# Kernel optimization log

Hardware: AMD Instinct MI355X
Metric: run time of the kernel (lower is better)

Reference implementation:

```python
import jax, jax.numpy as jnp
import numpy as np

DIM = 256
HEADS = 8
H = 32
W = 32
N = H * W  # must equal 4*DIM for the BatchNorm1d(dim*4) over the token dim to be valid
TAU = 2.0
V_TH = 1.0


def _rope_rotations():
    # RoPE buffer: shape (H, W, DIM//2) angles; k_max = DIM // (2*2)
    k_max = DIM // 4
    theta = 1.0 / (10000.0 ** (jnp.arange(k_max, dtype=jnp.float32) / k_max))
    hg, wg = jnp.meshgrid(jnp.arange(H, dtype=jnp.float32), jnp.arange(W, dtype=jnp.float32), indexing='ij')
    angles = jnp.concatenate([hg[..., None] * theta, wg[..., None] * theta], axis=-1)  # (H,W,DIM//2)
    return jnp.cos(angles), jnp.sin(angles)


def _apply_rope(x, cos, sin):
    # x: (b,H,W,DIM); complex rotation on consecutive (re,im) pairs
    x2 = x.reshape(*x.shape[:-1], -1, 2)
    re, im = x2[..., 0], x2[..., 1]
    out = jnp.stack([cos * re - sin * im, sin * re + cos * im], axis=-1)
    return out.reshape(x.shape)


def _lif(x):
    # MultiStepLIFNode(tau=2.0, detach_reset=True): time axis = axis 0 (here batch, as in source),
    # decay_input=True, v_reset=0 (hard reset), heaviside fwd + sigmoid(alpha=4) surrogate bwd.
    def step(v, xt):
        v = v + (xt - v) / TAU
        sg = jax.nn.sigmoid(4.0 * (v - V_TH))
        spike = jax.lax.stop_gradient((v >= V_TH).astype(x.dtype) - sg) + sg
        v = v * (1.0 - jax.lax.stop_gradient(spike))  # detach_reset hard reset to 0
        return v, spike
    _, s = jax.lax.scan(step, jnp.zeros_like(x[0]), x)
    return s


def setup_inputs() -> dict:
    key = jax.random.key(0)
    ks = jax.random.split(key, 4)
    x = jax.random.normal(ks[0], (8, N, DIM), dtype=jnp.float32)
    Wqk = jax.random.normal(ks[1], (DIM, 2 * DIM), dtype=jnp.float32) * 0.02
    bqk = jnp.zeros((2 * DIM,), dtype=jnp.float32)
    bn_gamma = jnp.ones((N,), dtype=jnp.float32)
    bn_beta = jnp.zeros((N,), dtype=jnp.float32)
    lepe_w = jax.random.normal(ks[2], (DIM, 1, 3, 3), dtype=jnp.float32) * 0.1
    lepe_b = jnp.zeros((DIM,), dtype=jnp.float32)
    return {"x": x, "Wqk": Wqk, "bqk": bqk, "bn_gamma": bn_gamma, "bn_beta": bn_beta,
            "lepe_w": lepe_w, "lepe_b": lepe_b}


def reference(x, Wqk, bqk, bn_gamma, bn_beta, lepe_w, lepe_b):
    b, n, c = x.shape
    hd = c // HEADS
    cos, sin = _rope_rotations()

    qk = x @ Wqk + bqk  # (b,n,2c)
    # Dropout is identity in eval. BatchNorm1d(4*dim) in eval mode: channels = token dim (n == 4*dim),
    # running_mean=0, running_var=1 -> pure affine per token index.
    qk = qk * bn_gamma[None, :, None] + bn_beta[None, :, None]
    qk = _lif(qk)
    q, k = qk[..., :c], qk[..., c:]  # reshape(b,n,2,c) split
    v = x
    q = jax.nn.elu(q) + 1.0
    k = jax.nn.elu(k) + 1.0

    q_rope = _apply_rope(q.reshape(b, H, W, c), cos, sin).reshape(b, n, HEADS, hd).transpose(0, 2, 1, 3)
    k_rope = _apply_rope(k.reshape(b, H, W, c), cos, sin).reshape(b, n, HEADS, hd).transpose(0, 2, 1, 3)
    qh = q.reshape(b, n, HEADS, hd).transpose(0, 2, 1, 3)  # (b,h,n,d)
    kh = k.reshape(b, n, HEADS, hd).transpose(0, 2, 1, 3)
    vh = v.reshape(b, n, HEADS, hd).transpose(0, 2, 1, 3)

    atten = jnp.einsum('bhnd,bhmd->bhnm', qh, kh)  # returned, not used for output
    kmean = kh.mean(axis=2, keepdims=True)  # (b,h,1,d)
    z = 1.0 / (jnp.einsum('bhnd,bhed->bhne', qh, kmean) + 1e-6)  # (b,h,n,1)
    kv = jnp.einsum('bhnd,bhne->bhde', k_rope, vh) / n  # (k^T n^-0.5) @ (v n^-0.5)
    out = jnp.einsum('bhnd,bhde->bhne', q_rope, kv) * z  # (b,h,n,d)
    out = out.transpose(0, 2, 1, 3).reshape(b, n, c)

    v_img = vh.transpose(0, 2, 1, 3).reshape(b, H, W, c).transpose(0, 3, 1, 2)  # (b,c,H,W)
    lepe = jax.lax.conv_general_dilated(v_img, lepe_w, (1, 1), 'SAME',
                                        feature_group_count=c,
                                        dimension_numbers=('NCHW', 'OIHW', 'NCHW'))
    lepe = lepe + lepe_b[None, :, None, None]
    out = out + lepe.transpose(0, 2, 3, 1).reshape(b, n, c)
    return (out, qh, kh, v_img, atten)
```

## Files before the change

### kernel.cpp

```cpp
#include <hip/hip_runtime.h>
#include <cstdint>
#include <cstddef>

#define OFF_OUT   0
#define OFF_QH    2097152
#define OFF_KH    4194304
#define OFF_VIMG  6291456
#define OFF_ATT   8388608

#define WS_MQ   0
#define WS_MK   65536
#define WS_TBL  131072
#define WS_KVP  393216
#define WS_KMP  655360

typedef float f32x4 __attribute__((ext_vector_type(4)));

__global__ __launch_bounds__(512) void phase1_kernel(
    const float* __restrict__ x, const float* __restrict__ Wqk,
    const float* __restrict__ bqk, const float* __restrict__ gamma,
    const float* __restrict__ beta, unsigned* __restrict__ mq,
    unsigned* __restrict__ mk, float* __restrict__ vimg,
    float* __restrict__ tbl)
{
    __shared__ float smem[12800];
    __shared__ unsigned nib[8][4][8][8];
    int t = threadIdx.x;
    int blk = blockIdx.x;

    if (blk >= 1536) {
        int id = (blk - 1536) * 512 + t;
        int j = id & 127, n = id >> 7;
        int i = (j < 64) ? j : j - 64;
        float th = powf(10000.0f, -(float)i * (1.0f / 64.0f));
        float pos = (float)((j < 64) ? (n >> 5) : (n & 31));
        float ang = pos * th;
        tbl[n * 256 + j * 2]     = cosf(ang);
        tbl[n * 256 + j * 2 + 1] = sinf(ang);
        return;
    }
    if (blk >= 512) {
        int tile = (blk - 512) * 2 + (t >> 8);
        int st = t & 255;
        float* s = smem + (t >> 8) * 1056;
        int b = tile >> 8, ti = tile & 255;
        int p0 = (ti >> 3) * 32, c0 = (ti & 7) * 32;
        int row = st >> 3, c4 = (st & 7) * 4;
        const float4 vl = *(const float4*)&x[(b * 1024 + p0 + row) * 256 + c0 + c4];
        s[row * 33 + c4 + 0] = vl.x; s[row * 33 + c4 + 1] = vl.y;
        s[row * 33 + c4 + 2] = vl.z; s[row * 33 + c4 + 3] = vl.w;
        __syncthreads();
        int cc = st >> 3, p4 = (st & 7) * 4;
        f32x4 o;
        o.x = s[(p4 + 0) * 33 + cc]; o.y = s[(p4 + 1) * 33 + cc];
        o.z = s[(p4 + 2) * 33 + cc]; o.w = s[(p4 + 3) * 33 + cc];
        __builtin_nontemporal_store(o, (f32x4*)&vimg[(b * 256 + c0 + cc) * 1024 + p0 + p4]);
        return;
    }

    int ks = t >> 8, tl = t & 255;
    int blk_n = blk >> 2, blk_c = blk & 3;
    int n0 = blk_n * 8, c0 = blk_c * 128;
    int c_t = tl & 31, n_l = tl >> 5;
    float* xs  = smem + ks * 2176;
    float* wsb = smem + 4352 + ks * 4224;

    float acc[8][4];
    #pragma unroll
    for (int b = 0; b < 8; ++b)
        #pragma unroll
        for (int j = 0; j < 4; ++j) acc[b][j] = 0.f;

    int um = tl >> 3, ukq = tl & 7;
    const float* gx1 = x + ((size_t)(um & 7) * 1024 + n0 + (um >> 3)) * 256 + ks * 128 + ukq * 4;
    const float* gx2 = gx1 + 4 * 256;
    float* lx1 = xs + (ukq * 4) * 68 + um;
    float* lx2 = lx1 + 32;
    const float* gw = Wqk + ((size_t)ks * 128 + (tl >> 5)) * 512 + c0 + (tl & 31) * 4;
    float* lw0 = wsb + (tl >> 5) * 132 + (tl & 31) * 4;

    f32x4 px0, px1, pw0, pw1, pw2, pw3;
    px0 = *(const f32x4*)(gx1);
    px1 = *(const f32x4*)(gx2);
    pw0 = *(const f32x4*)(gw);
    pw1 = *(const f32x4*)(gw + 8 * 512);
    pw2 = *(const f32x4*)(gw + 16 * 512);
    pw3 = *(const f32x4*)(gw + 24 * 512);

    for (int p = 0; p < 4; ++p) {
        #pragma unroll
        for (int j = 0; j < 4; ++j) { lx1[j * 68] = px0[j]; lx2[j * 68] = px1[j]; }
        *(f32x4*)(lw0)            = pw0;
        *(f32x4*)(lw0 + 8 * 132)  = pw1;
        *(f32x4*)(lw0 + 16 * 132) = pw2;
        *(f32x4*)(lw0 + 24 * 132) = pw3;
        __syncthreads();
        if (p < 3) {
            int ko = (p + 1) * 32;
            px0 = *(const f32x4*)(gx1 + ko);
            px1 = *(const f32x4*)(gx2 + ko);
            pw0 = *(const f32x4*)(gw + (ko + 0) * 512);
            pw1 = *(const f32x4*)(gw + (ko + 8) * 512);
            pw2 = *(const f32x4*)(gw + (ko + 16) * 512);
            pw3 = *(const f32x4*)(gw + (ko + 24) * 512);
        }
        #pragma unroll 8
        for (int kk = 0; kk < 32; ++kk) {
            f32x4 xa  = *(const f32x4*)(xs + kk * 68 + n_l * 8);
            f32x4 xb2 = *(const f32x4*)(xs + kk * 68 + n_l * 8 + 4);
            f32x4 w4  = *(const f32x4*)(wsb + kk * 132 + c_t * 4);
            #pragma unroll
            for (int b = 0; b < 4; ++b)
                #pragma unroll
                for (int j = 0; j < 4; ++j)
                    acc[b][j] = fmaf(xa[b], w4[j], acc[b][j]);
            #pragma unroll
            for (int b = 0; b < 4; ++b)
                #pragma unroll
                for (int j = 0; j < 4; ++j)
                    acc[b + 4][j] = fmaf(xb2[b], w4[j], acc[b + 4][j]);
        }
        __syncthreads();
    }

    float* comb = smem;
    if (ks == 1) {
        #pragma unroll
        for (int idx = 0; idx < 32; ++idx)
            comb[idx * 257 + tl] = acc[idx >> 2][idx & 3];
    }
    __syncthreads();
    if (ks == 0) {
        #pragma unroll
        for (int idx = 0; idx < 32; ++idx)
            acc[idx >> 2][idx & 3] += comb[idx * 257 + tl];
        float g = gamma[n0 + n_l], be = beta[n0 + n_l];
        f32x4 bq = *(const f32x4*)&bqk[c0 + c_t * 4];
        float v0 = 0.f, v1 = 0.f, v2 = 0.f, v3 = 0.f;
        #pragma unroll
        for (int b = 0; b < 8; ++b) {
            float a0 = (acc[b][0] + bq[0]) * g + be;
            float a1 = (acc[b][1] + bq[1]) * g + be;
            float a2 = (acc[b][2] + bq[2]) * g + be;
            float a3 = (acc[b][3] + bq[3]) * g + be;
            v0 = v0 + (a0 - v0) * 0.5f; v1 = v1 + (a1 - v1) * 0.5f;
            v2 = v2 + (a2 - v2) * 0.5f; v3 = v3 + (a3 - v3) * 0.5f;
            unsigned s0 = (v0 >= 1.f), s1 = (v1 >= 1.f), s2 = (v2 >= 1.f), s3 = (v3 >= 1.f);
            v0 = s0 ? 0.f : v0; v1 = s1 ? 0.f : v1;
            v2 = s2 ? 0.f : v2; v3 = s3 ? 0.f : v3;
            nib[n_l][c_t >> 3][c_t & 7][b] = s0 | (s1 << 1) | (s2 << 2) | (s3 << 3);
        }
    }
    __syncthreads();
    if (t < 256) {
        int b = t & 7, hp = (t >> 3) & 3, nl = t >> 5;
        unsigned wd = 0;
        #pragma unroll
        for (int c8 = 0; c8 < 8; ++c8)
            wd |= nib[nl][hp][c8][b] << (4 * c8);
        unsigned h = (unsigned)((blk_c & 1) * 4 + hp);
        unsigned* dst = (blk_c < 2) ? mq : mk;
        dst[b * 8192 + h * 1024 + n0 + nl] = wd;
    }
}

__global__ __launch_bounds__(256) void phase2_kernel(
    const unsigned* __restrict__ mq, const unsigned* __restrict__ mk,
    const float* __restrict__ x, const float* __restrict__ tbl,
    float* __restrict__ qh, float* __restrict__ kh, float* __restrict__ att,
    float* __restrict__ kvp, float* __restrict__ kmp)
{
    int t = threadIdx.x;
    if (blockIdx.x < 256) {
        int bh = blockIdx.x >> 2, seg = blockIdx.x & 3;
        int b = bh >> 3, h = bh & 7;
        int n0 = seg * 256;
        __shared__ float part[8][32];
        __shared__ float kr[64][36];
        __shared__ float vhs[64][33];
        int d = t & 31, ch = t >> 5;
        int sc = 0;
        for (int i = 0; i < 32; ++i)
            sc += (mk[bh * 1024 + n0 + ch * 32 + i] >> d) & 1u;
        part[ch][d] = (float)sc;
        __syncthreads();
        if (t < 32) {
            float cs = 0.f;
            #pragma unroll
            for (int j = 0; j < 8; ++j) cs += part[j][t];
            kmp[bh * 128 + seg * 32 + t] = cs;
        }
        float a0 = 0, a1 = 0, a2 = 0, a3 = 0;
        int e = t & 31, db = (t >> 5) * 4;
        for (int c0 = n0; c0 < n0 + 256; c0 += 64) {
            __syncthreads();
            #pragma unroll
            for (int i = 0; i < 8; ++i) {
                int f = t + i * 256;
                int nn = f >> 5, dd = f & 31;
                int n = c0 + nn;
                unsigned w = mk[bh * 1024 + n];
                float kd = 1.0f + (float)((w >> dd) & 1u);
                float ko = 1.0f + (float)((w >> (dd ^ 1)) & 1u);
                const float* cp = tbl + n * 256 + h * 32 + (dd & ~1);
                float cc2 = cp[0], ss2 = cp[1];
                kr[nn][dd] = (dd & 1) ? (ss2 * ko + cc2 * kd) : (cc2 * kd - ss2 * ko);
                vhs[nn][dd] = x[(b * 1024 + n) * 256 + h * 32 + dd];
            }
            __syncthreads();
            #pragma unroll 8
            for (int nn = 0; nn < 64; ++nn) {
                float ve = vhs[nn][e];
                float4 kk = *(const float4*)&kr[nn][db];
                a0 = fmaf(kk.x, ve, a0); a1 = fmaf(kk.y, ve, a1);
                a2 = fmaf(kk.z, ve, a2); a3 = fmaf(kk.w, ve, a3);
            }
        }
        float* dst = kvp + bh * 4096 + seg * 1024;
        dst[(db + 0) * 32 + e] = a0;
        dst[(db + 1) * 32 + e] = a1;
        dst[(db + 2) * 32 + e] = a2;
        dst[(db + 3) * 32 + e] = a3;
        return;
    }
    int blk = blockIdx.x - 256;
    int bh = blk >> 5;
    int tile = blk & 31;
    {
        int row = tile * 32 + (t >> 3);
        int d0 = (t & 7) * 4;
        unsigned wq = mq[bh * 1024 + row], wk = mk[bh * 1024 + row];
        f32x4 a, bb;
        a.x = 1.f + (float)((wq >> (d0 + 0)) & 1u);
        a.y = 1.f + (float)((wq >> (d0 + 1)) & 1u);
        a.z = 1.f + (float)((wq >> (d0 + 2)) & 1u);
        a.w = 1.f + (float)((wq >> (d0 + 3)) & 1u);
        bb.x = 1.f + (float)((wk >> (d0 + 0)) & 1u);
        bb.y = 1.f + (float)((wk >> (d0 + 1)) & 1u);
        bb.z = 1.f + (float)((wk >> (d0 + 2)) & 1u);
        bb.w = 1.f + (float)((wk >> (d0 + 3)) & 1u);
        __builtin_nontemporal_store(a,  (f32x4*)&qh[((bh * 1024 + row) << 5) + d0]);
        __builtin_nontemporal_store(bb, (f32x4*)&kh[((bh * 1024 + row) << 5) + d0]);
    }
    uint4 mm = ((const uint4*)(mk + bh * 1024))[t];
    float4 rr;
    rr.x = (float)__popc(mm.x); rr.y = (float)__popc(mm.y);
    rr.z = (float)__popc(mm.z); rr.w = (float)__popc(mm.w);
    float* base = att + ((size_t)bh * 1024 + (size_t)tile * 32) * 1024;
    for (int row = 0; row < 32; ++row) {
        unsigned mqw = mq[bh * 1024 + tile * 32 + row];
        float rq = 32.0f + (float)__popc(mqw);
        f32x4 o;
        o.x = rq + rr.x + (float)__popc(mqw & mm.x);
        o.y = rq + rr.y + (float)__popc(mqw & mm.y);
        o.z = rq + rr.z + (float)__popc(mqw & mm.z);
        o.w = rq + rr.w + (float)__popc(mqw & mm.w);
        __builtin_nontemporal_store(o, (f32x4*)(base + (size_t)row * 1024) + t);
    }
}

__global__ __launch_bounds__(256) void out_kernel(
    const unsigned* __restrict__ mq, const float* __restrict__ x,
    const float* __restrict__ tbl, const float* __restrict__ kvp,
    const float* __restrict__ kmp, const float* __restrict__ lw,
    const float* __restrict__ lb, float* __restrict__ out)
{
    int t = threadIdx.x;
    int bi = blockIdx.x;
    int bh = bi >> 3, sub = bi & 7;
    int pseg = sub >> 1, half = sub & 1;
    int b = bh >> 3, h = bh & 7;
    bool hy = (h < 4);
    int e = t & 31, p_l = t >> 5;
    int p = pseg * 8 + p_l;
    int q0 = half * 16;

    __shared__ float kvs[32][32];
    __shared__ float kmf[32];
    __shared__ float zs[128];
    const float inv = 1.0f / 1024.0f;
    #pragma unroll
    for (int i = 0; i < 4; ++i) {
        int f = t + i * 256;
        const float* kp = kvp + bh * 4096 + f;
        kvs[f >> 5][f & 31] = (kp[0] + kp[1024] + kp[2048] + kp[3072]) * inv;
    }
    if (t < 32) {
        const float* mp = kmp + bh * 128 + t;
        kmf[t] = 1.0f + (mp[0] + mp[32] + mp[64] + mp[96]) * inv;
    }
    __syncthreads();
    float S = 0.f;
    #pragma unroll
    for (int dd = 0; dd < 32; ++dd) S += kmf[dd];
    if (t < 128) {
        int pl2 = t >> 4, iq = t & 15;
        int pp = pseg * 8 + pl2, qq = q0 + iq;
        int n = hy ? (pp * 32 + qq) : (qq * 32 + pp);
        unsigned w = mq[bh * 1024 + n];
        float acc = S;
        #pragma unroll
        for (int dd = 0; dd < 32; ++dd)
            acc += (float)((w >> dd) & 1u) * kmf[dd];
        zs[t] = 1.0f / (acc + 1e-6f);
    }
    int n_ref = hy ? (p * 32) : p;
    const float* cp = tbl + n_ref * 256 + h * 32;
    float E[16], O[16], B = 0.f;
    #pragma unroll
    for (int j = 0; j < 16; ++j) {
        float c2 = cp[2 * j], s2 = cp[2 * j + 1];
        float K0 = kvs[2 * j][e], K1 = kvs[2 * j + 1][e];
        E[j] = c2 * K0 + s2 * K1;
        O[j] = c2 * K1 - s2 * K0;
        B += E[j] + O[j];
    }
    __syncthreads();
    int c = h * 32 + e;
    float w9[9];
    #pragma unroll
    for (int j = 0; j < 9; ++j) w9[j] = lw[c * 9 + j];
    float lbv = lb[c];
    const float* xb = x + (size_t)b * 262144 + c;
    auto ld = [&](int yy, int xx) -> float {
        if ((unsigned)yy > 31u || (unsigned)xx > 31u) return 0.f;
        return xb[(yy * 32 + xx) * 256];
    };
    if (hy) {
        int y = p;
        float Wm0 = ld(y - 1, q0 - 1), Wm1 = ld(y, q0 - 1), Wm2 = ld(y + 1, q0 - 1);
        float Wc0 = ld(y - 1, q0),     Wc1 = ld(y, q0),     Wc2 = ld(y + 1, q0);
        #pragma unroll 4
        for (int i = 0; i < 16; ++i) {
            int m = q0 + i;
            float Wp0 = ld(y - 1, m + 1), Wp1 = ld(y, m + 1), Wp2 = ld(y + 1, m + 1);
            int n = y * 32 + m;
            unsigned w = mq[bh * 1024 + n];
            float o = B;
            #pragma unroll
            for (int j = 0; j < 16; ++j) {
                o += (float)((w >> (2 * j)) & 1u) * E[j];
                o += (float)((w >> (2 * j + 1)) & 1u) * O[j];
            }
            o *= zs[p_l * 16 + i];
            float l = lbv;
            l = fmaf(w9[0], Wm0, l); l = fmaf(w9[1], Wc0, l); l = fmaf(w9[2], Wp0, l);
            l = fmaf(w9[3], Wm1, l); l = fmaf(w9[4], Wc1, l); l = fmaf(w9[5], Wp1, l);
            l = fmaf(w9[6], Wm2, l); l = fmaf(w9[7], Wc2, l); l = fmaf(w9[8], Wp2, l);
            __builtin_nontemporal_store(o + l, &out[((b * 1024 + n) << 8) + c]);
            Wm0 = Wc0; Wm1 = Wc1; Wm2 = Wc2;
            Wc0 = Wp0; Wc1 = Wp1; Wc2 = Wp2;
        }
    } else {
        int xx0 = p;
        float Wm0 = ld(q0 - 1, xx0 - 1), Wm1 = ld(q0 - 1, xx0), Wm2 = ld(q0 - 1, xx0 + 1);
        float Wc0 = ld(q0, xx0 - 1),     Wc1 = ld(q0, xx0),     Wc2 = ld(q0, xx0 + 1);
        #pragma unroll 4
        for (int i = 0; i < 16; ++i) {
            int m = q0 + i;
            float Wp0 = ld(m + 1, xx0 - 1), Wp1 = ld(m + 1, xx0), Wp2 = ld(m + 1, xx0 + 1);
            int n = m * 32 + xx0;
            unsigned w = mq[bh * 1024 + n];
            float o = B;
            #pragma unroll
            for (int j = 0; j < 16; ++j) {
                o += (float)((w >> (2 * j)) & 1u) * E[j];
                o += (float)((w >> (2 * j + 1)) & 1u) * O[j];
            }
            o *= zs[p_l * 16 + i];
            float l = lbv;
            l = fmaf(w9[0], Wm0, l); l = fmaf(w9[1], Wm1, l); l = fmaf(w9[2], Wm2, l);
            l = fmaf(w9[3], Wc0, l); l = fmaf(w9[4], Wc1, l); l = fmaf(w9[5], Wc2, l);
            l = fmaf(w9[6], Wp0, l); l = fmaf(w9[7], Wp1, l); l = fmaf(w9[8], Wp2, l);
            __builtin_nontemporal_store(o + l, &out[((b * 1024 + n) << 8) + c]);
            Wm0 = Wc0; Wm1 = Wc1; Wm2 = Wc2;
            Wc0 = Wp0; Wc1 = Wp1; Wc2 = Wp2;
        }
    }
}

extern "C" void kernel_launch(void* const* d_in, const int* in_sizes, int n_in,
                              void* d_out, int out_size, void* d_ws, size_t ws_size,
                              hipStream_t stream)
{
    const float* x     = (const float*)d_in[0];
    const float* Wqk   = (const float*)d_in[1];
    const float* bqk   = (const float*)d_in[2];
    const float* gamma = (const float*)d_in[3];
    const float* beta  = (const float*)d_in[4];
    const float* lw    = (const float*)d_in[5];
    const float* lb    = (const float*)d_in[6];
    float* out = (float*)d_out;
    unsigned* ws = (unsigned*)d_ws;
    unsigned* mq = ws + WS_MQ;
    unsigned* mk = ws + WS_MK;
    float* tbl  = (float*)(ws + WS_TBL);
    float* kvp  = (float*)(ws + WS_KVP);
    float* kmp  = (float*)(ws + WS_KMP);

    hipLaunchKernelGGL(phase1_kernel, dim3(1792), dim3(512), 0, stream,
                       x, Wqk, bqk, gamma, beta, mq, mk, out + OFF_VIMG, tbl);
    hipLaunchKernelGGL(phase2_kernel, dim3(2304), dim3(256), 0, stream,
                       mq, mk, x, tbl, out + OFF_QH, out + OFF_KH, out + OFF_ATT,
                       kvp, kmp);
    hipLaunchKernelGGL(out_kernel, dim3(512), dim3(256), 0, stream,
                       mq, x, tbl, kvp, kmp, lw, lb, out + OFF_OUT);
}
```

Before: 107.6 us.

## Reschedule kernels so K-mask GEMM runs first and Q GEMM overlaps KV reduction

The original first kernel computed both the Q and K spike masks, the RoPE table and the v_img transpose. Now phase A computes only the K half of the GEMM/LIF alongside the table and the transpose. Phase B computes the Q half concurrently with the KV/k-mean partial reductions, which need only the K mask. The attention-matrix/qh/kh writes are then fused into the same launch as the final output kernel. The aim is to fill idle CUs by pairing independent work in each launch, at the cost of heavier mixed blocks and a different load balance.

```diff
diff --git a/kernel.cpp b/kernel.cpp
--- a/kernel.cpp
+++ b/kernel.cpp
@@ -16,50 +16,14 @@
 
 typedef float f32x4 __attribute__((ext_vector_type(4)));
 
-__global__ __launch_bounds__(512) void phase1_kernel(
+__device__ __forceinline__ void gemm_lif_512(
     const float* __restrict__ x, const float* __restrict__ Wqk,
     const float* __restrict__ bqk, const float* __restrict__ gamma,
     const float* __restrict__ beta, unsigned* __restrict__ mq,
-    unsigned* __restrict__ mk, float* __restrict__ vimg,
-    float* __restrict__ tbl)
+    unsigned* __restrict__ mk, float* smem, unsigned* nib,
+    int blk_n, int blk_c, int t)
 {
-    __shared__ float smem[12800];
-    __shared__ unsigned nib[8][4][8][8];
-    int t = threadIdx.x;
-    int blk = blockIdx.x;
-
-    if (blk >= 1536) {
-        int id = (blk - 1536) * 512 + t;
-        int j = id & 127, n = id >> 7;
-        int i = (j < 64) ? j : j - 64;
-        float th = powf(10000.0f, -(float)i * (1.0f / 64.0f));
-        float pos = (float)((j < 64) ? (n >> 5) : (n & 31));
-        float ang = pos * th;
-        tbl[n * 256 + j * 2]     = cosf(ang);
-        tbl[n * 256 + j * 2 + 1] = sinf(ang);
-        return;
-    }
-    if (blk >= 512) {
-        int tile = (blk - 512) * 2 + (t >> 8);
-        int st = t & 255;
-        float* s = smem + (t >> 8) * 1056;
-        int b = tile >> 8, ti = tile & 255;
-        int p0 = (ti >> 3) * 32, c0 = (ti & 7) * 32;
-        int row = st >> 3, c4 = (st & 7) * 4;
-        const float4 vl = *(const float4*)&x[(b * 1024 + p0 + row) * 256 + c0 + c4];
-        s[row * 33 + c4 + 0] = vl.x; s[row * 33 + c4 + 1] = vl.y;
-        s[row * 33 + c4 + 2] = vl.z; s[row * 33 + c4 + 3] = vl.w;
-        __syncthreads();
-        int cc = st >> 3, p4 = (st & 7) * 4;
-        f32x4 o;
-        o.x = s[(p4 + 0) * 33 + cc]; o.y = s[(p4 + 1) * 33 + cc];
-        o.z = s[(p4 + 2) * 33 + cc]; o.w = s[(p4 + 3) * 33 + cc];
-        __builtin_nontemporal_store(o, (f32x4*)&vimg[(b * 256 + c0 + cc) * 1024 + p0 + p4]);
-        return;
-    }
-
     int ks = t >> 8, tl = t & 255;
-    int blk_n = blk >> 2, blk_c = blk & 3;
     int n0 = blk_n * 8, c0 = blk_c * 128;
     int c_t = tl & 31, n_l = tl >> 5;
     float* xs  = smem + ks * 2176;
@@ -148,7 +112,8 @@
             unsigned s0 = (v0 >= 1.f), s1 = (v1 >= 1.f), s2 = (v2 >= 1.f), s3 = (v3 >= 1.f);
             v0 = s0 ? 0.f : v0; v1 = s1 ? 0.f : v1;
             v2 = s2 ? 0.f : v2; v3 = s3 ? 0.f : v3;
-            nib[n_l][c_t >> 3][c_t & 7][b] = s0 | (s1 << 1) | (s2 << 2) | (s3 << 3);
+            nib[n_l * 256 + (c_t >> 3) * 64 + (c_t & 7) * 8 + b] =
+                s0 | (s1 << 1) | (s2 << 2) | (s3 << 3);
         }
     }
     __syncthreads();
@@ -157,115 +122,174 @@
         unsigned wd = 0;
         #pragma unroll
         for (int c8 = 0; c8 < 8; ++c8)
-            wd |= nib[nl][hp][c8][b] << (4 * c8);
+            wd |= nib[nl * 256 + hp * 64 + c8 * 8 + b] << (4 * c8);
         unsigned h = (unsigned)((blk_c & 1) * 4 + hp);
         unsigned* dst = (blk_c < 2) ? mq : mk;
         dst[b * 8192 + h * 1024 + n0 + nl] = wd;
     }
 }
 
-__global__ __launch_bounds__(256) void phase2_kernel(
+__global__ __launch_bounds__(512) void phaseA_kernel(
+    const float* __restrict__ x, const float* __restrict__ Wqk,
+    const float* __restrict__ bqk, const float* __restrict__ gamma,
+    const float* __restrict__ beta, unsigned* __restrict__ mq,
+    unsigned* __restrict__ mk, float* __restrict__ vimg,
+    float* __restrict__ tbl)
+{
+    __shared__ float smem[12800];
+    __shared__ unsigned nib[2048];
+    int t = threadIdx.x;
+    int blk = blockIdx.x;
+    if (blk < 256) {
+        gemm_lif_512(x, Wqk, bqk, gamma, beta, mq, mk, smem, nib,
+                     blk >> 1, 2 + (blk & 1), t);
+        return;
+    }
+    if (blk >= 1280) {
+        int id = (blk - 1280) * 512 + t;
+        int j = id & 127, n = id >> 7;
+        int i = (j < 64) ? j : j - 64;
+        float th = powf(10000.0f, -(float)i * (1.0f / 64.0f));
+        float pos = (float)((j < 64) ? (n >> 5) : (n & 31));
+        float ang = pos * th;
+        tbl[n * 256 + j * 2]     = cosf(ang);
+        tbl[n * 256 + j * 2 + 1] = sinf(ang);
+        return;
+    }
+    int tile = (blk - 256) * 2 + (t >> 8);
+    int st = t & 255;
+    float* s = smem + (t >> 8) * 1056;
+    int b = tile >> 8, ti = tile & 255;
+    int p0 = (ti >> 3) * 32, c0 = (ti & 7) * 32;
+    int row = st >> 3, c4 = (st & 7) * 4;
+    const float4 vl = *(const float4*)&x[(b * 1024 + p0 + row) * 256 + c0 + c4];
+    s[row * 33 + c4 + 0] = vl.x; s[row * 33 + c4 + 1] = vl.y;
+    s[row * 33 + c4 + 2] = vl.z; s[row * 33 + c4 + 3] = vl.w;
+    __syncthreads();
+    int cc = st >> 3, p4 = (st & 7) * 4;
+    f32x4 o;
+    o.x = s[(p4 + 0) * 33 + cc]; o.y = s[(p4 + 1) * 33 + cc];
+    o.z = s[(p4 + 2) * 33 + cc]; o.w = s[(p4 + 3) * 33 + cc];
+    __builtin_nontemporal_store(o, (f32x4*)&vimg[(b * 256 + c0 + cc) * 1024 + p0 + p4]);
+}
+
+__global__ __launch_bounds__(512) void phaseB_kernel(
+    const float* __restrict__ x, const float* __restrict__ Wqk,
+    const float* __restrict__ bqk, const float* __restrict__ gamma,
+    const float* __restrict__ beta, unsigned* __restrict__ mq,
+    unsigned* __restrict__ mk, const float* __restrict__ tbl,
+    float* __restrict__ kvp, float* __restrict__ kmp)
+{
+    __shared__ float smem[12800];
+    __shared__ unsigned nib[2048];
+    int t = threadIdx.x;
+    int blk = blockIdx.x;
+    if (blk < 256) {
+        gemm_lif_512(x, Wqk, bqk, gamma, beta, mq, mk, smem, nib,
+                     blk >> 1, blk & 1, t);
+        return;
+    }
+    int ks2 = t >> 8, tl = t & 255;
+    int unit = (blk - 256) * 2 + ks2;
+    int bh = unit >> 2, seg = unit & 3;
+    int b = bh >> 3, h = bh & 7;
+    int n0 = seg * 256;
+    float* kr   = smem + ks2 * 4800;
+    float* vhs  = kr + 2304;
+    float* part = kr + 4416;
+    int d = tl & 31, ch = tl >> 5;
+    int sc = 0;
+    for (int i = 0; i < 32; ++i)
+        sc += (mk[bh * 1024 + n0 + ch * 32 + i] >> d) & 1u;
+    part[ch * 32 + d] = (float)sc;
+    __syncthreads();
+    if (tl < 32) {
+        float cs = 0.f;
+        #pragma unroll
+        for (int j = 0; j < 8; ++j) cs += part[j * 32 + tl];
+        kmp[bh * 128 + seg * 32 + tl] = cs;
+    }
+    float a0 = 0, a1 = 0, a2 = 0, a3 = 0;
+    int e = tl & 31, db = (tl >> 5) * 4;
+    for (int c0 = n0; c0 < n0 + 256; c0 += 64) {
+        __syncthreads();
+        #pragma unroll
+        for (int i = 0; i < 8; ++i) {
+            int f = tl + i * 256;
+            int nn = f >> 5, dd = f & 31;
+            int n = c0 + nn;
+            unsigned w = mk[bh * 1024 + n];
+            float kd = 1.0f + (float)((w >> dd) & 1u);
+            float ko = 1.0f + (float)((w >> (dd ^ 1)) & 1u);
+            const float* cp = tbl + n * 256 + h * 32 + (dd & ~1);
+            float cc2 = cp[0], ss2 = cp[1];
+            kr[nn * 36 + dd] = (dd & 1) ? (ss2 * ko + cc2 * kd) : (cc2 * kd - ss2 * ko);
+            vhs[nn * 33 + dd] = x[(b * 1024 + n) * 256 + h * 32 + dd];
+        }
+        __syncthreads();
+        #pragma unroll 8
+        for (int nn = 0; nn < 64; ++nn) {
+            float ve = vhs[nn * 33 + e];
+            float4 kk = *(const float4*)&kr[nn * 36 + db];
+            a0 = fmaf(kk.x, ve, a0); a1 = fmaf(kk.y, ve, a1);
+            a2 = fmaf(kk.z, ve, a2); a3 = fmaf(kk.w, ve, a3);
+        }
+    }
+    float* dst = kvp + bh * 4096 + seg * 1024;
+    dst[(db + 0) * 32 + e] = a0;
+    dst[(db + 1) * 32 + e] = a1;
+    dst[(db + 2) * 32 + e] = a2;
+    dst[(db + 3) * 32 + e] = a3;
+}
+
+__global__ __launch_bounds__(256) void phaseC_kernel(
     const unsigned* __restrict__ mq, const unsigned* __restrict__ mk,
     const float* __restrict__ x, const float* __restrict__ tbl,
-    float* __restrict__ qh, float* __restrict__ kh, float* __restrict__ att,
-    float* __restrict__ kvp, float* __restrict__ kmp)
+    const float* __restrict__ kvp, const float* __restrict__ kmp,
+    const float* __restrict__ lw, const float* __restrict__ lb,
+    float* __restrict__ outbase)
 {
     int t = threadIdx.x;
-    if (blockIdx.x < 256) {
-        int bh = blockIdx.x >> 2, seg = blockIdx.x & 3;
-        int b = bh >> 3, h = bh & 7;
-        int n0 = seg * 256;
-        __shared__ float part[8][32];
-        __shared__ float kr[64][36];
-        __shared__ float vhs[64][33];
-        int d = t & 31, ch = t >> 5;
-        int sc = 0;
-        for (int i = 0; i < 32; ++i)
-            sc += (mk[bh * 1024 + n0 + ch * 32 + i] >> d) & 1u;
-        part[ch][d] = (float)sc;
-        __syncthreads();
-        if (t < 32) {
-            float cs = 0.f;
-            #pragma unroll
-            for (int j = 0; j < 8; ++j) cs += part[j][t];
-            kmp[bh * 128 + seg * 32 + t] = cs;
-        }
-        float a0 = 0, a1 = 0, a2 = 0, a3 = 0;
-        int e = t & 31, db = (t >> 5) * 4;
-        for (int c0 = n0; c0 < n0 + 256; c0 += 64) {
-            __syncthreads();
-            #pragma unroll
-            for (int i = 0; i < 8; ++i) {
-                int f = t + i * 256;
-                int nn = f >> 5, dd = f & 31;
-                int n = c0 + nn;
-                unsigned w = mk[bh * 1024 + n];
-                float kd = 1.0f + (float)((w >> dd) & 1u);
-                float ko = 1.0f + (float)((w >> (dd ^ 1)) & 1u);
-                const float* cp = tbl + n * 256 + h * 32 + (dd & ~1);
-                float cc2 = cp[0], ss2 = cp[1];
-                kr[nn][dd] = (dd & 1) ? (ss2 * ko + cc2 * kd) : (cc2 * kd - ss2 * ko);
-                vhs[nn][dd] = x[(b * 1024 + n) * 256 + h * 32 + dd];
-            }
-            __syncthreads();
-            #pragma unroll 8
-            for (int nn = 0; nn < 64; ++nn) {
-                float ve = vhs[nn][e];
-                float4 kk = *(const float4*)&kr[nn][db];
-                a0 = fmaf(kk.x, ve, a0); a1 = fmaf(kk.y, ve, a1);
-                a2 = fmaf(kk.z, ve, a2); a3 = fmaf(kk.w, ve, a3);
-            }
-        }
-        float* dst = kvp + bh * 4096 + seg * 1024;
-        dst[(db + 0) * 32 + e] = a0;
-        dst[(db + 1) * 32 + e] = a1;
-        dst[(db + 2) * 32 + e] = a2;
-        dst[(db + 3) * 32 + e] = a3;
+    if (blockIdx.x >= 512) {
+        int blk = blockIdx.x - 512;
+        int bh = blk >> 5;
+        int tile = blk & 31;
+        float* qh = outbase + OFF_QH;
+        float* kh = outbase + OFF_KH;
+        float* att = outbase + OFF_ATT;
+        {
+            int row = tile * 32 + (t >> 3);
+            int d0 = (t & 7) * 4;
+            unsigned wq = mq[bh * 1024 + row], wk = mk[bh * 1024 + row];
+            f32x4 a, bb;
+            a.x = 1.f + (float)((wq >> (d0 + 0)) & 1u);
+            a.y = 1.f + (float)((wq >> (d0 + 1)) & 1u);
+            a.z = 1.f + (float)((wq >> (d0 + 2)) & 1u);
+            a.w = 1.f + (float)((wq >> (d0 + 3)) & 1u);
+            bb.x = 1.f + (float)((wk >> (d0 + 0)) & 1u);
+            bb.y = 1.f + (float)((wk >> (d0 + 1)) & 1u);
+            bb.z = 1.f + (float)((wk >> (d0 + 2)) & 1u);
+            bb.w = 1.f + (float)((wk >> (d0 + 3)) & 1u);
+            __builtin_nontemporal_store(a,  (f32x4*)&qh[((bh * 1024 + row) << 5) + d0]);
+            __builtin_nontemporal_store(bb, (f32x4*)&kh[((bh * 1024 + row) << 5) + d0]);
+        }
+        uint4 mm = ((const uint4*)(mk + bh * 1024))[t];
+        float4 rr;
+        rr.x = (float)__popc(mm.x); rr.y = (float)__popc(mm.y);
+        rr.z = (float)__popc(mm.z); rr.w = (float)__popc(mm.w);
+        float* base = att + ((size_t)bh * 1024 + (size_t)tile * 32) * 1024;
+        for (int row = 0; row < 32; ++row) {
+            unsigned mqw = mq[bh * 1024 + tile * 32 + row];
+            float rq = 32.0f + (float)__popc(mqw);
+            f32x4 o;
+            o.x = rq + rr.x + (float)__popc(mqw & mm.x);
+            o.y = rq + rr.y + (float)__popc(mqw & mm.y);
+            o.z = rq + rr.z + (float)__popc(mqw & mm.z);
+            o.w = rq + rr.w + (float)__popc(mqw & mm.w);
+            __builtin_nontemporal_store(o, (f32x4*)(base + (size_t)row * 1024) + t);
+        }
         return;
     }
-    int blk = blockIdx.x - 256;
-    int bh = blk >> 5;
-    int tile = blk & 31;
-    {
-        int row = tile * 32 + (t >> 3);
-        int d0 = (t & 7) * 4;
-        unsigned wq = mq[bh * 1024 + row], wk = mk[bh * 1024 + row];
-        f32x4 a, bb;
-        a.x = 1.f + (float)((wq >> (d0 + 0)) & 1u);
-        a.y = 1.f + (float)((wq >> (d0 + 1)) & 1u);
-        a.z = 1.f + (float)((wq >> (d0 + 2)) & 1u);
-        a.w = 1.f + (float)((wq >> (d0 + 3)) & 1u);
-        bb.x = 1.f + (float)((wk >> (d0 + 0)) & 1u);
-        bb.y = 1.f + (float)((wk >> (d0 + 1)) & 1u);
-        bb.z = 1.f + (float)((wk >> (d0 + 2)) & 1u);
-        bb.w = 1.f + (float)((wk >> (d0 + 3)) & 1u);
-        __builtin_nontemporal_store(a,  (f32x4*)&qh[((bh * 1024 + row) << 5) + d0]);
-        __builtin_nontemporal_store(bb, (f32x4*)&kh[((bh * 1024 + row) << 5) + d0]);
-    }
-    uint4 mm = ((const uint4*)(mk + bh * 1024))[t];
-    float4 rr;
-    rr.x = (float)__popc(mm.x); rr.y = (float)__popc(mm.y);
-    rr.z = (float)__popc(mm.z); rr.w = (float)__popc(mm.w);
-    float* base = att + ((size_t)bh * 1024 + (size_t)tile * 32) * 1024;
-    for (int row = 0; row < 32; ++row) {
-        unsigned mqw = mq[bh * 1024 + tile * 32 + row];
-        float rq = 32.0f + (float)__popc(mqw);
-        f32x4 o;
-        o.x = rq + rr.x + (float)__popc(mqw & mm.x);
-        o.y = rq + rr.y + (float)__popc(mqw & mm.y);
-        o.z = rq + rr.z + (float)__popc(mqw & mm.z);
-        o.w = rq + rr.w + (float)__popc(mqw & mm.w);
-        __builtin_nontemporal_store(o, (f32x4*)(base + (size_t)row * 1024) + t);
-    }
-}
-
-__global__ __launch_bounds__(256) void out_kernel(
-    const unsigned* __restrict__ mq, const float* __restrict__ x,
-    const float* __restrict__ tbl, const float* __restrict__ kvp,
-    const float* __restrict__ kmp, const float* __restrict__ lw,
-    const float* __restrict__ lb, float* __restrict__ out)
-{
-    int t = threadIdx.x;
     int bi = blockIdx.x;
     int bh = bi >> 3, sub = bi & 7;
     int pseg = sub >> 1, half = sub & 1;
@@ -274,6 +298,7 @@
     int e = t & 31, p_l = t >> 5;
     int p = pseg * 8 + p_l;
     int q0 = half * 16;
+    float* out = outbase + OFF_OUT;
 
     __shared__ float kvs[32][32];
     __shared__ float kmf[32];
@@ -398,11 +423,10 @@
     float* kvp  = (float*)(ws + WS_KVP);
     float* kmp  = (float*)(ws + WS_KMP);
 
-    hipLaunchKernelGGL(phase1_kernel, dim3(1792), dim3(512), 0, stream,
+    hipLaunchKernelGGL(phaseA_kernel, dim3(1536), dim3(512), 0, stream,
                        x, Wqk, bqk, gamma, beta, mq, mk, out + OFF_VIMG, tbl);
-    hipLaunchKernelGGL(phase2_kernel, dim3(2304), dim3(256), 0, stream,
-                       mq, mk, x, tbl, out + OFF_QH, out + OFF_KH, out + OFF_ATT,
-                       kvp, kmp);
-    hipLaunchKernelGGL(out_kernel, dim3(512), dim3(256), 0, stream,
-                       mq, x, tbl, kvp, kmp, lw, lb, out + OFF_OUT);
+    hipLaunchKernelGGL(phaseB_kernel, dim3(384), dim3(512), 0, stream,
+                       x, Wqk, bqk, gamma, beta, mq, mk, tbl, kvp, kmp);
+    hipLaunchKernelGGL(phaseC_kernel, dim3(2560), dim3(256), 0, stream,
+                       mq, mk, x, tbl, kvp, kmp, lw, lb, out);
 }
```

Result: faster. 102.2 us (-5.0%).
